# Optimization experiments

Measured on AMD Instinct MI355X. Metric: run time of the kernel, lower is better.

The kernel has to match this reference:

```python
import jax, jax.numpy as jnp
import numpy as np

N_NODES = 100000
N_EDGES = 400000
N_GRAPHS = 2000
IN_DIM = 58
HEADS = 4
HID = 64           # per-head hidden = output_dim // heads = 256 // 4
OUT = 256
NEG_SLOPE = 0.2    # PyG GATConv default


def _glorot(key, shape):
    fan_in, fan_out = shape[0], shape[-1]
    lim = jnp.sqrt(6.0 / (fan_in + fan_out)).astype(jnp.float32)
    return jax.random.uniform(key, shape, jnp.float32, -lim, lim)


def setup_inputs() -> dict:
    key = jax.random.key(0)
    ks = jax.random.split(key, 16)
    x = jax.random.normal(ks[0], (N_NODES, IN_DIM), jnp.float32)
    edge_index = jax.random.randint(ks[1], (2, N_EDGES), 0, N_NODES, jnp.int64)
    batch = jnp.sort(jax.random.randint(ks[2], (N_NODES,), 0, N_GRAPHS, jnp.int64))
    return {
        "x": x,
        "edge_index": edge_index,
        "batch": batch,
        # layer 1: 58 -> 4 heads x 64, concat -> 256
        "W1": _glorot(ks[3], (IN_DIM, HEADS * HID)),
        "a_src1": _glorot(ks[4], (HEADS, HID)),
        "a_dst1": _glorot(ks[5], (HEADS, HID)),
        "b1": jnp.zeros((HEADS * HID,), jnp.float32),
        # layer 2: 256 -> 4 heads x 64, concat -> 256
        "W2": _glorot(ks[6], (HEADS * HID, HEADS * HID)),
        "a_src2": _glorot(ks[7], (HEADS, HID)),
        "a_dst2": _glorot(ks[8], (HEADS, HID)),
        "b2": jnp.zeros((HEADS * HID,), jnp.float32),
        # layer 3: 256 -> 1 head x 256, no concat (mean over 1 head)
        "W3": _glorot(ks[9], (HEADS * HID, OUT)),
        "a_src3": _glorot(ks[10], (1, OUT)),
        "a_dst3": _glorot(ks[11], (1, OUT)),
        "b3": jnp.zeros((OUT,), jnp.float32),
    }


def _gat_layer(x, src, dst, W, a_src, a_dst, b, heads, ch, concat):
    n = x.shape[0]
    h = (x @ W).reshape(n, heads, ch)                      # [N,H,C]
    e_src = jnp.einsum("nhc,hc->nh", h, a_src)             # [N,H]
    e_dst = jnp.einsum("nhc,hc->nh", h, a_dst)
    e = jax.nn.leaky_relu(e_src[src] + e_dst[dst], NEG_SLOPE)  # [E,H]
    # segment softmax over destination nodes (self-loops ensure non-empty segments)
    m = jax.ops.segment_max(e, dst, num_segments=n)
    ex = jnp.exp(e - m[dst])
    denom = jax.ops.segment_sum(ex, dst, num_segments=n)
    coef = ex / denom[dst]                                 # [E,H]
    out = jax.ops.segment_sum(h[src] * coef[:, :, None], dst, num_segments=n)
    out = out.reshape(n, heads * ch) if concat else out.mean(axis=1)
    return out + b


def reference(x, edge_index, batch, W1, a_src1, a_dst1, b1,
              W2, a_src2, a_dst2, b2, W3, a_src3, a_dst3, b3):
    n = x.shape[0]
    loops = jnp.arange(n, dtype=edge_index.dtype)
    src = jnp.concatenate([edge_index[0], loops])          # add_self_loops (PyG default)
    dst = jnp.concatenate([edge_index[1], loops])
    h = jax.nn.relu(_gat_layer(x, src, dst, W1, a_src1, a_dst1, b1, HEADS, HID, True))
    h = jax.nn.relu(_gat_layer(h, src, dst, W2, a_src2, a_dst2, b2, HEADS, HID, True))
    h = _gat_layer(h, src, dst, W3, a_src3, a_dst3, b3, 1, OUT, False)
    # global max pool over graphs
    return jax.ops.segment_max(h, batch, num_segments=N_GRAPHS)
```

## Files before the change

### kernel.cpp

```cpp
#include <hip/hip_runtime.h>
#include <hip/hip_bf16.h>
#include <math.h>

#define N_NODES_C 100000
#define E_ORIG    400000
#define E_TOT     500000
#define N_GRAPHS_C 2000
#define KDIM      256

typedef __attribute__((ext_vector_type(8))) short short8v;
typedef __attribute__((ext_vector_type(4))) float f32x4;

__device__ __forceinline__ void gload_lds16(const void* g, void* l) {
    __builtin_amdgcn_global_load_lds(
        (const __attribute__((address_space(1))) unsigned int*)g,
        (__attribute__((address_space(3))) unsigned int*)l, 16, 0, 0);
}

__device__ __forceinline__ float bflo(unsigned u) { return __uint_as_float(u << 16); }
__device__ __forceinline__ float bfhi(unsigned u) { return __uint_as_float(u & 0xffff0000u); }

__global__ void count_deg_k(const int* __restrict__ ei, int* __restrict__ deg) {
    int e = blockIdx.x * 256 + threadIdx.x;
    if (e >= E_TOT) return;
    int d = (e < E_ORIG) ? ei[E_ORIG + e] : (e - E_ORIG);
    atomicAdd(&deg[d], 1);
}

__global__ void scan_chunk(const int* __restrict__ in, int* __restrict__ out,
                           int* __restrict__ partials, int n) {
    __shared__ int s[256];
    int tid = threadIdx.x;
    int i = blockIdx.x * 256 + tid;
    int v = (i < n) ? in[i] : 0;
    s[tid] = v;
    __syncthreads();
    for (int off = 1; off < 256; off <<= 1) {
        int t = (tid >= off) ? s[tid - off] : 0;
        __syncthreads();
        s[tid] += t;
        __syncthreads();
    }
    if (i < n) out[i] = s[tid] - v;
    if (tid == 255) partials[blockIdx.x] = s[255];
}

__global__ void scan_partials(int* p, int nb) {
    __shared__ int s[512];
    int tid = threadIdx.x;
    int v = (tid < nb) ? p[tid] : 0;
    s[tid] = v;
    __syncthreads();
    for (int off = 1; off < 512; off <<= 1) {
        int t = (tid >= off) ? s[tid - off] : 0;
        __syncthreads();
        s[tid] += t;
        __syncthreads();
    }
    if (tid < nb) p[tid] = s[tid] - v;
}

__global__ void add_partials(int* out, const int* __restrict__ p, int n) {
    int i = blockIdx.x * 256 + threadIdx.x;
    if (i < n) out[i] += p[blockIdx.x];
}

__global__ void scatter_k(const int* __restrict__ ei, const int* __restrict__ rowoff,
                          int* cursor, int* __restrict__ csr_src,
                          int* __restrict__ csr_dst) {
    int e = blockIdx.x * 256 + threadIdx.x;
    if (e >= E_TOT) return;
    int s, d;
    if (e < E_ORIG) { s = ei[e]; d = ei[E_ORIG + e]; }
    else            { s = e - E_ORIG; d = s; }
    int pos = rowoff[d] + atomicAdd(&cursor[d], 1);
    csr_src[pos] = s;
    csr_dst[pos] = d;
}

__global__ void conv_x_k(const float* __restrict__ x, __hip_bfloat16* __restrict__ Xb) {
    int idx = blockIdx.x * 256 + threadIdx.x;
    if (idx >= N_NODES_C * 64) return;
    int row = idx >> 6, c = idx & 63;
    float v = (c < 58) ? x[row * 58 + c] : 0.f;
    Xb[idx] = __float2bfloat16(v);
}

template <int K, int KPAD>
__global__ void conv_wt_k(const float* __restrict__ W, __hip_bfloat16* __restrict__ Wt) {
    int idx = blockIdx.x * 256 + threadIdx.x;
    if (idx >= 256 * KPAD) return;
    int c = idx / KPAD, k = idx - c * KPAD;
    float v = (k < K) ? W[k * 256 + c] : 0.f;
    Wt[idx] = __float2bfloat16(v);
}

template <int KPAD, int NH>
__global__ __launch_bounds__(256) void gemm_mfma(
        const __hip_bfloat16* __restrict__ Xb, const __hip_bfloat16* __restrict__ Wt,
        const float* __restrict__ ASRC, const float* __restrict__ ADST,
        __hip_bfloat16* __restrict__ H, float* __restrict__ ES, float* __restrict__ ED) {
    __shared__ char As[64 * 128];
    __shared__ char Bs[256 * 128];
    __shared__ float red[2][64][2];

    const int t = threadIdx.x;
    const int wv = t >> 6, lane = t & 63;
    const int wr = wv >> 1, wc = wv & 1;
    const int r15 = lane & 15, hi = lane >> 4;
    const int n0 = blockIdx.x * 64;
    const int srow = lane >> 3;
    const int sx = ((lane & 7) ^ srow) * 16;
    constexpr int KB = KPAD * 2;

    f32x4 acc[2][8];
#pragma unroll
    for (int m = 0; m < 2; m++)
#pragma unroll
        for (int n = 0; n < 8; n++) acc[m][n] = (f32x4){0.f, 0.f, 0.f, 0.f};

    for (int kt = 0; kt < KPAD / 64; kt++) {
        if (kt) __syncthreads();
        const int k0b = kt * 128;
#pragma unroll
        for (int p = 0; p < 2; p++) {
            int i = wv * 2 + p;
            int gr = n0 + i * 8 + srow;
            if (gr > N_NODES_C - 1) gr = N_NODES_C - 1;
            gload_lds16((const char*)Xb + (size_t)gr * KB + k0b + sx, As + i * 1024);
        }
#pragma unroll
        for (int p = 0; p < 8; p++) {
            int i = wv * 8 + p;
            int col = i * 8 + srow;
            gload_lds16((const char*)Wt + (size_t)col * KB + k0b + sx, Bs + i * 1024);
        }
        asm volatile("s_waitcnt vmcnt(0)" ::: "memory");
        __syncthreads();

#pragma unroll
        for (int ks = 0; ks < 2; ks++) {
            const int cx = ((ks * 4 + hi) ^ (r15 & 7)) * 16;
            short8v a0 = *(const short8v*)(As + (wr * 32 + 0  + r15) * 128 + cx);
            short8v a1 = *(const short8v*)(As + (wr * 32 + 16 + r15) * 128 + cx);
            short8v b[8];
#pragma unroll
            for (int n = 0; n < 8; n++)
                b[n] = *(const short8v*)(Bs + (wc * 128 + n * 16 + r15) * 128 + cx);
#pragma unroll
            for (int n = 0; n < 8; n++) {
                acc[0][n] = __builtin_amdgcn_mfma_f32_16x16x32_bf16(a0, b[n], acc[0][n], 0, 0, 0);
                acc[1][n] = __builtin_amdgcn_mfma_f32_16x16x32_bf16(a1, b[n], acc[1][n], 0, 0, 0);
            }
        }
    }

    float asv[8], adv[8];
#pragma unroll
    for (int n = 0; n < 8; n++) {
        int col = wc * 128 + n * 16 + r15;
        asv[n] = ASRC[col];
        adv[n] = ADST[col];
    }

#pragma unroll
    for (int m = 0; m < 2; m++) {
#pragma unroll
        for (int j = 0; j < 4; j++) {
            int lrow = wr * 32 + m * 16 + hi * 4 + j;
            int row = n0 + lrow;
            bool ok = row < N_NODES_C;
            if (ok) {
#pragma unroll
                for (int n = 0; n < 8; n++)
                    H[(size_t)row * KDIM + wc * 128 + n * 16 + r15] =
                        __float2bfloat16(acc[m][n][j]);
            }
            if (NH == 4) {
                float p0s = 0.f, p1s = 0.f, p0d = 0.f, p1d = 0.f;
#pragma unroll
                for (int n = 0; n < 4; n++) {
                    p0s = fmaf(acc[m][n][j], asv[n], p0s);
                    p0d = fmaf(acc[m][n][j], adv[n], p0d);
                    p1s = fmaf(acc[m][n + 4][j], asv[n + 4], p1s);
                    p1d = fmaf(acc[m][n + 4][j], adv[n + 4], p1d);
                }
#pragma unroll
                for (int s = 8; s; s >>= 1) {
                    p0s += __shfl_xor(p0s, s, 16);
                    p0d += __shfl_xor(p0d, s, 16);
                    p1s += __shfl_xor(p1s, s, 16);
                    p1d += __shfl_xor(p1d, s, 16);
                }
                if (r15 == 0 && ok) {
                    ES[row * 4 + wc * 2 + 0] = p0s;
                    ES[row * 4 + wc * 2 + 1] = p1s;
                    ED[row * 4 + wc * 2 + 0] = p0d;
                    ED[row * 4 + wc * 2 + 1] = p1d;
                }
            } else {
                float ps = 0.f, pd = 0.f;
#pragma unroll
                for (int n = 0; n < 8; n++) {
                    ps = fmaf(acc[m][n][j], asv[n], ps);
                    pd = fmaf(acc[m][n][j], adv[n], pd);
                }
#pragma unroll
                for (int s = 8; s; s >>= 1) {
                    ps += __shfl_xor(ps, s, 16);
                    pd += __shfl_xor(pd, s, 16);
                }
                if (r15 == 0) { red[0][lrow][wc] = ps; red[1][lrow][wc] = pd; }
            }
        }
    }
    if (NH == 1) {
        __syncthreads();
        if (t < 64) {
            int row = n0 + t;
            if (row < N_NODES_C) {
                ES[row] = red[0][t][0] + red[0][t][1];
                ED[row] = red[1][t][0] + red[1][t][1];
            }
        }
    }
}

template <int NH>
__global__ __launch_bounds__(256) void edge_e_k(
        const int* __restrict__ csr_src, const int* __restrict__ csr_dst,
        const float* __restrict__ ES, const float* __restrict__ ED,
        float* __restrict__ E) {
    int j = blockIdx.x * 256 + threadIdx.x;
    if (j >= E_TOT) return;
    int s = csr_src[j], d = csr_dst[j];
    if (NH == 4) {
        float4 es = *(const float4*)&ES[s * 4];
        float4 ed = *(const float4*)&ED[d * 4];
        float4 e;
        e.x = es.x + ed.x; e.x = (e.x > 0.f) ? e.x : 0.2f * e.x;
        e.y = es.y + ed.y; e.y = (e.y > 0.f) ? e.y : 0.2f * e.y;
        e.z = es.z + ed.z; e.z = (e.z > 0.f) ? e.z : 0.2f * e.z;
        e.w = es.w + ed.w; e.w = (e.w > 0.f) ? e.w : 0.2f * e.w;
        *(float4*)&E[j * 4] = e;
    } else {
        float e = ES[s] + ED[d];
        E[j] = (e > 0.f) ? e : 0.2f * e;
    }
}

template <int NH, bool RELU>
__global__ __launch_bounds__(256) void agg_kernel(
        const __hip_bfloat16* __restrict__ H, const int* __restrict__ rowoff,
        const int* __restrict__ csr_src, const float* __restrict__ E,
        const float* __restrict__ bias, __hip_bfloat16* __restrict__ Out) {
    int node = blockIdx.x * 8 + (threadIdx.x >> 5);
    int l = threadIdx.x & 31;
    int c0 = l * 8;
    int head = (NH == 4) ? (l >> 3) : 0;
    int beg = rowoff[node], end = rowoff[node + 1];

    float m = -1e30f;
    for (int j = beg; j < end; j++) m = fmaxf(m, E[j * NH + head]);

    float s = 0.f;
    float a[8];
#pragma unroll
    for (int i = 0; i < 8; i++) a[i] = 0.f;
    const unsigned short* Hu = (const unsigned short*)H;

#define ACC8(v, p) \
    a[0] = fmaf(p, bflo(v.x), a[0]); a[1] = fmaf(p, bfhi(v.x), a[1]); \
    a[2] = fmaf(p, bflo(v.y), a[2]); a[3] = fmaf(p, bfhi(v.y), a[3]); \
    a[4] = fmaf(p, bflo(v.z), a[4]); a[5] = fmaf(p, bfhi(v.z), a[5]); \
    a[6] = fmaf(p, bflo(v.w), a[6]); a[7] = fmaf(p, bfhi(v.w), a[7]);

    int j = beg;
    for (; j + 2 <= end; j += 2) {
        int s0 = csr_src[j], s1 = csr_src[j + 1];
        float e0 = E[j * NH + head], e1 = E[(j + 1) * NH + head];
        uint4 v0 = *(const uint4*)(Hu + (size_t)s0 * KDIM + c0);
        uint4 v1 = *(const uint4*)(Hu + (size_t)s1 * KDIM + c0);
        float p0 = __expf(e0 - m), p1 = __expf(e1 - m);
        s += p0 + p1;
        ACC8(v0, p0)
        ACC8(v1, p1)
    }
    if (j < end) {
        int s0 = csr_src[j];
        float e0 = E[j * NH + head];
        uint4 v0 = *(const uint4*)(Hu + (size_t)s0 * KDIM + c0);
        float p0 = __expf(e0 - m);
        s += p0;
        ACC8(v0, p0)
    }
#undef ACC8

    float inv = 1.f / s;
    float4 b0 = *(const float4*)&bias[c0];
    float4 b1 = *(const float4*)&bias[c0 + 4];
    float o[8];
    o[0] = fmaf(a[0], inv, b0.x); o[1] = fmaf(a[1], inv, b0.y);
    o[2] = fmaf(a[2], inv, b0.z); o[3] = fmaf(a[3], inv, b0.w);
    o[4] = fmaf(a[4], inv, b1.x); o[5] = fmaf(a[5], inv, b1.y);
    o[6] = fmaf(a[6], inv, b1.z); o[7] = fmaf(a[7], inv, b1.w);
    __hip_bfloat16 rb[8];
#pragma unroll
    for (int i = 0; i < 8; i++) {
        float v = RELU ? fmaxf(o[i], 0.f) : o[i];
        rb[i] = __float2bfloat16(v);
    }
    *(uint4*)&Out[(size_t)node * KDIM + c0] = *(uint4*)rb;
}

__global__ __launch_bounds__(256) void pool_k(
        const __hip_bfloat16* __restrict__ O, const int* __restrict__ batch,
        float* __restrict__ out) {
    __shared__ int range[2];
    int g = blockIdx.x, k = threadIdx.x;
    if (k < 2) {
        int v = g + k;
        int lo = 0, hi = N_NODES_C;
        while (lo < hi) { int mid = (lo + hi) >> 1; if (batch[mid] < v) lo = mid + 1; else hi = mid; }
        range[k] = lo;
    }
    __syncthreads();
    float m = -INFINITY;
    for (int i = range[0]; i < range[1]; i++)
        m = fmaxf(m, __bfloat162float(O[(size_t)i * KDIM + k]));
    out[(size_t)g * KDIM + k] = m;
}

extern "C" void kernel_launch(void* const* d_in, const int* in_sizes, int n_in,
                              void* d_out, int out_size, void* d_ws, size_t ws_size,
                              hipStream_t stream) {
    const float* x     = (const float*)d_in[0];
    const int*   ei    = (const int*)d_in[1];
    const int*   batch = (const int*)d_in[2];
    const float* W1  = (const float*)d_in[3];
    const float* as1 = (const float*)d_in[4];
    const float* ad1 = (const float*)d_in[5];
    const float* b1  = (const float*)d_in[6];
    const float* W2  = (const float*)d_in[7];
    const float* as2 = (const float*)d_in[8];
    const float* ad2 = (const float*)d_in[9];
    const float* b2  = (const float*)d_in[10];
    const float* W3  = (const float*)d_in[11];
    const float* as3 = (const float*)d_in[12];
    const float* ad3 = (const float*)d_in[13];
    const float* b3  = (const float*)d_in[14];
    float* out = (float*)d_out;

    char* p = (char*)d_ws;
    auto alloc = [&](size_t bytes) { char* r = p; p += (bytes + 255) & ~(size_t)255; return r; };
    __hip_bfloat16* Xb  = (__hip_bfloat16*)alloc((size_t)N_NODES_C * 64 * 2);
    __hip_bfloat16* Hb  = (__hip_bfloat16*)alloc((size_t)N_NODES_C * KDIM * 2);
    __hip_bfloat16* Nb  = (__hip_bfloat16*)alloc((size_t)N_NODES_C * KDIM * 2);
    __hip_bfloat16* Wt1 = (__hip_bfloat16*)alloc(256 * 64 * 2);
    __hip_bfloat16* Wt2 = (__hip_bfloat16*)alloc(256 * 256 * 2);
    __hip_bfloat16* Wt3 = (__hip_bfloat16*)alloc(256 * 256 * 2);
    float* ES     = (float*)alloc((size_t)N_NODES_C * 4 * 4);
    float* ED     = (float*)alloc((size_t)N_NODES_C * 4 * 4);
    float* Ecoef  = (float*)alloc((size_t)E_TOT * 4 * 4);
    int* deg      = (int*)alloc((N_NODES_C + 1) * 4);
    int* rowoff   = (int*)alloc((N_NODES_C + 1) * 4);
    int* cursor   = (int*)alloc(N_NODES_C * 4);
    int* csr      = (int*)alloc((size_t)E_TOT * 4);
    int* csrd     = (int*)alloc((size_t)E_TOT * 4);
    int* partials = (int*)alloc(512 * 4);

    conv_x_k<<<(N_NODES_C * 64 + 255) / 256, 256, 0, stream>>>(x, Xb);
    conv_wt_k<58, 64><<<64, 256, 0, stream>>>(W1, Wt1);
    conv_wt_k<256, 256><<<256, 256, 0, stream>>>(W2, Wt2);
    conv_wt_k<256, 256><<<256, 256, 0, stream>>>(W3, Wt3);

    hipMemsetAsync(deg, 0, (N_NODES_C + 1) * 4, stream);
    hipMemsetAsync(cursor, 0, N_NODES_C * 4, stream);
    int egrid = (E_TOT + 255) / 256;
    count_deg_k<<<egrid, 256, 0, stream>>>(ei, deg);
    int nb = (N_NODES_C + 1 + 255) / 256;
    scan_chunk<<<nb, 256, 0, stream>>>(deg, rowoff, partials, N_NODES_C + 1);
    scan_partials<<<1, 512, 0, stream>>>(partials, nb);
    add_partials<<<nb, 256, 0, stream>>>(rowoff, partials, N_NODES_C + 1);
    scatter_k<<<egrid, 256, 0, stream>>>(ei, rowoff, cursor, csr, csrd);

    int ggrid = (N_NODES_C + 63) / 64;
    int agrid = N_NODES_C / 8;
    gemm_mfma<64, 4><<<ggrid, 256, 0, stream>>>(Xb, Wt1, as1, ad1, Hb, ES, ED);
    edge_e_k<4><<<egrid, 256, 0, stream>>>(csr, csrd, ES, ED, Ecoef);
    agg_kernel<4, true><<<agrid, 256, 0, stream>>>(Hb, rowoff, csr, Ecoef, b1, Nb);
    gemm_mfma<256, 4><<<ggrid, 256, 0, stream>>>(Nb, Wt2, as2, ad2, Hb, ES, ED);
    edge_e_k<4><<<egrid, 256, 0, stream>>>(csr, csrd, ES, ED, Ecoef);
    agg_kernel<4, true><<<agrid, 256, 0, stream>>>(Hb, rowoff, csr, Ecoef, b2, Nb);
    gemm_mfma<256, 1><<<ggrid, 256, 0, stream>>>(Nb, Wt3, as3, ad3, Hb, ES, ED);
    edge_e_k<1><<<egrid, 256, 0, stream>>>(csr, csrd, ES, ED, Ecoef);
    agg_kernel<1, false><<<agrid, 256, 0, stream>>>(Hb, rowoff, csr, Ecoef, b3, Nb);
    pool_k<<<N_GRAPHS_C, 256, 0, stream>>>(Nb, batch, out);
}
```

Baseline: 357.5 us.

## Enlarge GEMM row tile, unroll aggregation by four, vectorize graph pooling

```diff
diff --git a/kernel.cpp b/kernel.cpp
--- a/kernel.cpp
+++ b/kernel.cpp
@@ -96,26 +96,26 @@
 }
 
 template <int KPAD, int NH>
-__global__ __launch_bounds__(256) void gemm_mfma(
+__global__ __launch_bounds__(256, 2) void gemm_mfma(
         const __hip_bfloat16* __restrict__ Xb, const __hip_bfloat16* __restrict__ Wt,
         const float* __restrict__ ASRC, const float* __restrict__ ADST,
         __hip_bfloat16* __restrict__ H, float* __restrict__ ES, float* __restrict__ ED) {
-    __shared__ char As[64 * 128];
+    __shared__ char As[128 * 128];
     __shared__ char Bs[256 * 128];
-    __shared__ float red[2][64][2];
+    __shared__ float red[2][128][2];
 
     const int t = threadIdx.x;
     const int wv = t >> 6, lane = t & 63;
     const int wr = wv >> 1, wc = wv & 1;
     const int r15 = lane & 15, hi = lane >> 4;
-    const int n0 = blockIdx.x * 64;
+    const int n0 = blockIdx.x * 128;
     const int srow = lane >> 3;
     const int sx = ((lane & 7) ^ srow) * 16;
     constexpr int KB = KPAD * 2;
 
-    f32x4 acc[2][8];
-#pragma unroll
-    for (int m = 0; m < 2; m++)
+    f32x4 acc[4][8];
+#pragma unroll
+    for (int m = 0; m < 4; m++)
 #pragma unroll
         for (int n = 0; n < 8; n++) acc[m][n] = (f32x4){0.f, 0.f, 0.f, 0.f};
 
@@ -123,8 +123,8 @@
         if (kt) __syncthreads();
         const int k0b = kt * 128;
 #pragma unroll
-        for (int p = 0; p < 2; p++) {
-            int i = wv * 2 + p;
+        for (int p = 0; p < 4; p++) {
+            int i = wv * 4 + p;
             int gr = n0 + i * 8 + srow;
             if (gr > N_NODES_C - 1) gr = N_NODES_C - 1;
             gload_lds16((const char*)Xb + (size_t)gr * KB + k0b + sx, As + i * 1024);
@@ -141,16 +141,16 @@
 #pragma unroll
         for (int ks = 0; ks < 2; ks++) {
             const int cx = ((ks * 4 + hi) ^ (r15 & 7)) * 16;
-            short8v a0 = *(const short8v*)(As + (wr * 32 + 0  + r15) * 128 + cx);
-            short8v a1 = *(const short8v*)(As + (wr * 32 + 16 + r15) * 128 + cx);
-            short8v b[8];
-#pragma unroll
-            for (int n = 0; n < 8; n++)
-                b[n] = *(const short8v*)(Bs + (wc * 128 + n * 16 + r15) * 128 + cx);
+            short8v a[4];
+#pragma unroll
+            for (int m = 0; m < 4; m++)
+                a[m] = *(const short8v*)(As + (wr * 64 + m * 16 + r15) * 128 + cx);
 #pragma unroll
             for (int n = 0; n < 8; n++) {
-                acc[0][n] = __builtin_amdgcn_mfma_f32_16x16x32_bf16(a0, b[n], acc[0][n], 0, 0, 0);
-                acc[1][n] = __builtin_amdgcn_mfma_f32_16x16x32_bf16(a1, b[n], acc[1][n], 0, 0, 0);
+                short8v b = *(const short8v*)(Bs + (wc * 128 + n * 16 + r15) * 128 + cx);
+#pragma unroll
+                for (int m = 0; m < 4; m++)
+                    acc[m][n] = __builtin_amdgcn_mfma_f32_16x16x32_bf16(a[m], b, acc[m][n], 0, 0, 0);
             }
         }
     }
@@ -164,10 +164,10 @@
     }
 
 #pragma unroll
-    for (int m = 0; m < 2; m++) {
+    for (int m = 0; m < 4; m++) {
 #pragma unroll
         for (int j = 0; j < 4; j++) {
-            int lrow = wr * 32 + m * 16 + hi * 4 + j;
+            int lrow = wr * 64 + m * 16 + hi * 4 + j;
             int row = n0 + lrow;
             bool ok = row < N_NODES_C;
             if (ok) {
@@ -216,7 +216,7 @@
     }
     if (NH == 1) {
         __syncthreads();
-        if (t < 64) {
+        if (t < 128) {
             int row = n0 + t;
             if (row < N_NODES_C) {
                 ES[row] = red[0][t][0] + red[0][t][1];
@@ -276,17 +276,23 @@
     a[6] = fmaf(p, bflo(v.w), a[6]); a[7] = fmaf(p, bfhi(v.w), a[7]);
 
     int j = beg;
-    for (; j + 2 <= end; j += 2) {
-        int s0 = csr_src[j], s1 = csr_src[j + 1];
-        float e0 = E[j * NH + head], e1 = E[(j + 1) * NH + head];
+    for (; j + 4 <= end; j += 4) {
+        int s0 = csr_src[j], s1 = csr_src[j + 1], s2 = csr_src[j + 2], s3 = csr_src[j + 3];
+        float e0 = E[(j + 0) * NH + head], e1 = E[(j + 1) * NH + head];
+        float e2 = E[(j + 2) * NH + head], e3 = E[(j + 3) * NH + head];
         uint4 v0 = *(const uint4*)(Hu + (size_t)s0 * KDIM + c0);
         uint4 v1 = *(const uint4*)(Hu + (size_t)s1 * KDIM + c0);
+        uint4 v2 = *(const uint4*)(Hu + (size_t)s2 * KDIM + c0);
+        uint4 v3 = *(const uint4*)(Hu + (size_t)s3 * KDIM + c0);
         float p0 = __expf(e0 - m), p1 = __expf(e1 - m);
-        s += p0 + p1;
+        float p2 = __expf(e2 - m), p3 = __expf(e3 - m);
+        s += p0 + p1 + p2 + p3;
         ACC8(v0, p0)
         ACC8(v1, p1)
-    }
-    if (j < end) {
+        ACC8(v2, p2)
+        ACC8(v3, p3)
+    }
+    for (; j < end; j++) {
         int s0 = csr_src[j];
         float e0 = E[j * NH + head];
         uint4 v0 = *(const uint4*)(Hu + (size_t)s0 * KDIM + c0);
@@ -317,6 +323,7 @@
         const __hip_bfloat16* __restrict__ O, const int* __restrict__ batch,
         float* __restrict__ out) {
     __shared__ int range[2];
+    __shared__ float red[3][256];
     int g = blockIdx.x, k = threadIdx.x;
     if (k < 2) {
         int v = g + k;
@@ -325,10 +332,28 @@
         range[k] = lo;
     }
     __syncthreads();
-    float m = -INFINITY;
-    for (int i = range[0]; i < range[1]; i++)
-        m = fmaxf(m, __bfloat162float(O[(size_t)i * KDIM + k]));
-    out[(size_t)g * KDIM + k] = m;
+    int cg = k & 63;
+    int ro = k >> 6;
+    float m0 = -INFINITY, m1 = -INFINITY, m2 = -INFINITY, m3 = -INFINITY;
+    const unsigned short* Ou = (const unsigned short*)O;
+    for (int i = range[0] + ro; i < range[1]; i += 4) {
+        uint2 v = *(const uint2*)(Ou + (size_t)i * KDIM + cg * 4);
+        m0 = fmaxf(m0, bflo(v.x)); m1 = fmaxf(m1, bfhi(v.x));
+        m2 = fmaxf(m2, bflo(v.y)); m3 = fmaxf(m3, bfhi(v.y));
+    }
+    if (ro) {
+        red[ro - 1][cg * 4 + 0] = m0; red[ro - 1][cg * 4 + 1] = m1;
+        red[ro - 1][cg * 4 + 2] = m2; red[ro - 1][cg * 4 + 3] = m3;
+    }
+    __syncthreads();
+    if (ro == 0) {
+        m0 = fmaxf(fmaxf(m0, red[0][cg * 4 + 0]), fmaxf(red[1][cg * 4 + 0], red[2][cg * 4 + 0]));
+        m1 = fmaxf(fmaxf(m1, red[0][cg * 4 + 1]), fmaxf(red[1][cg * 4 + 1], red[2][cg * 4 + 1]));
+        m2 = fmaxf(fmaxf(m2, red[0][cg * 4 + 2]), fmaxf(red[1][cg * 4 + 2], red[2][cg * 4 + 2]));
+        m3 = fmaxf(fmaxf(m3, red[0][cg * 4 + 3]), fmaxf(red[1][cg * 4 + 3], red[2][cg * 4 + 3]));
+        float4 o = make_float4(m0, m1, m2, m3);
+        *(float4*)&out[(size_t)g * KDIM + cg * 4] = o;
+    }
 }
 
 extern "C" void kernel_launch(void* const* d_in, const int* in_sizes, int n_in,
@@ -365,7 +390,7 @@
     int* deg      = (int*)alloc((N_NODES_C + 1) * 4);
     int* rowoff   = (int*)alloc((N_NODES_C + 1) * 4);
     int* cursor   = (int*)alloc(N_NODES_C * 4);
-    int* csr      = (int*)alloc((size_t)E_TOT * 4);
+    int* csr      = (int*)alloc((size_t)E_TOT * 4 + 256);
     int* csrd     = (int*)alloc((size_t)E_TOT * 4);
     int* partials = (int*)alloc(512 * 4);
 
@@ -384,7 +409,7 @@
     add_partials<<<nb, 256, 0, stream>>>(rowoff, partials, N_NODES_C + 1);
     scatter_k<<<egrid, 256, 0, stream>>>(ei, rowoff, cursor, csr, csrd);
 
-    int ggrid = (N_NODES_C + 63) / 64;
+    int ggrid = (N_NODES_C + 127) / 128;
     int agrid = N_NODES_C / 8;
     gemm_mfma<64, 4><<<ggrid, 256, 0, stream>>>(Xb, Wt1, as1, ad1, Hb, ES, ED);
     edge_e_k<4><<<egrid, 256, 0, stream>>>(csr, csrd, ES, ED, Ecoef);
```

Result: faster. 341.7 us (-4.4%).
